# Performance work log

Measured on AMD Instinct MI355X. Metric: run time of the kernel, lower is better.

The kernel has to match this reference:

```python
import jax, jax.numpy as jnp
import numpy as np

D_MODEL = 1024
NUM_HEADS = 16
D_K = D_MODEL // NUM_HEADS
ROPE_BASE = 10000.0


def _rotate_half(x):
    # interleaved pairs: (x0, x1) -> (-x1, x0)
    x1 = x[..., ::2]
    x2 = x[..., 1::2]
    return jnp.stack((-x2, x1), axis=-1).reshape(x.shape)


def _rope(q, k):
    seq_len = q.shape[-2]
    freqs = ROPE_BASE ** (jnp.arange(0, D_K, 2, dtype=q.dtype) / D_K)  # [D_K/2]
    angles = jnp.arange(seq_len, dtype=q.dtype)[:, None] / freqs[None, :]  # [S, D_K/2]
    sin = jnp.repeat(jnp.sin(angles), 2, axis=-1)[None, None]  # [1,1,S,D_K]
    cos = jnp.repeat(jnp.cos(angles), 2, axis=-1)[None, None]
    return q * cos + _rotate_half(q) * sin, k * cos + _rotate_half(k) * sin


def setup_inputs() -> dict:
    key = jax.random.key(0)
    ks = jax.random.split(key, 9)
    B, S, D = 2, 2048, D_MODEL
    s = 1.0 / np.sqrt(D)
    inp = {
        "x": jax.random.normal(ks[0], (B, S, D), dtype=jnp.float32),
        "wq": jax.random.uniform(ks[1], (D, D), jnp.float32, -s, s),
        "bq": jax.random.uniform(ks[2], (D,), jnp.float32, -s, s),
        "wk": jax.random.uniform(ks[3], (D, D), jnp.float32, -s, s),
        "bk": jax.random.uniform(ks[4], (D,), jnp.float32, -s, s),
        "wv": jax.random.uniform(ks[5], (D, D), jnp.float32, -s, s),
        "bv": jax.random.uniform(ks[6], (D,), jnp.float32, -s, s),
        "wo": jax.random.uniform(ks[7], (D, D), jnp.float32, -s, s),
        "bo": jax.random.uniform(ks[8], (D,), jnp.float32, -s, s),
    }
    return inp


def reference(x, wq, bq, wk, bk, wv, bv, wo, bo):
    B, S, D = x.shape
    H, dk = NUM_HEADS, D_K
    # torch Linear: y = x @ W.T + b
    Q = (x @ wq.T + bq).reshape(B, S, H, dk).transpose(0, 2, 1, 3)  # [B,H,S,dk]
    K = (x @ wk.T + bk).reshape(B, S, H, dk).transpose(0, 2, 1, 3)
    V = (x @ wv.T + bv).reshape(B, S, H, dk).transpose(0, 2, 1, 3)
    Q, K = _rope(Q, K)
    score = jnp.einsum("bhqd,bhkd->bhqk", Q, K) / jnp.sqrt(jnp.asarray(dk, x.dtype))
    attn_w = jax.nn.softmax(score, axis=-1)
    out = jnp.einsum("bhqk,bhkd->bhqd", attn_w, V)  # [B,H,S,dk]
    out = out.transpose(0, 2, 1, 3).reshape(B, S, D)
    return out @ wo.T + bo
```

## Files before the change

kernel.cpp:

```cpp
#include <hip/hip_runtime.h>
#include <hip/hip_bf16.h>
#include <math.h>

typedef __bf16 bf16_t;
typedef __bf16 bf16x4_t __attribute__((ext_vector_type(4)));
typedef __bf16 bf16x8_t __attribute__((ext_vector_type(8)));
typedef float  f32x4_t  __attribute__((ext_vector_type(4)));

#define SEQ 2048
#define DM  1024
#define NH  16
#define DK  64
#define ROPE_C 0.4152410118609203f
#define EXP_C (1.4426950408889634f / 8.0f)

#define GLD16(gp, lp) \
  __builtin_amdgcn_global_load_lds((__attribute__((address_space(1))) const void*)(gp), \
                                   (__attribute__((address_space(3))) void*)(lp), 16, 0, 0)

__global__ __launch_bounds__(256)
void prep_kernel(const float* __restrict__ x,  const float* __restrict__ wq,
                 const float* __restrict__ wk, const float* __restrict__ wv,
                 const float* __restrict__ wo, bf16_t* __restrict__ dst,
                 float2* __restrict__ lut) {
  if (blockIdx.x < 8192) {
    int i = blockIdx.x * 256 + threadIdx.x;
    const float* s;
    if (i < 1048576) {
      s = x + (size_t)i * 4;
    } else {
      int j = i - 1048576;
      int w = j >> 18;
      const float* base = (w == 0) ? wq : (w == 1) ? wk : (w == 2) ? wv : wo;
      s = base + (size_t)(j & 262143) * 4;
    }
    float4 v = *(const float4*)s;
    bf16x4_t o;
    o.x = (bf16_t)v.x; o.y = (bf16_t)v.y; o.z = (bf16_t)v.z; o.w = (bf16_t)v.w;
    ((bf16x4_t*)dst)[i] = o;
  } else {
    int i = (blockIdx.x - 8192) * 256 + threadIdx.x;
    int s = i >> 5, f = i & 31;
    float ang = (float)s * exp2f(-ROPE_C * (float)f);
    float sn, cs;
    sincosf(ang, &sn, &cs);
    lut[i] = make_float2(sn, cs);
  }
}

__global__ __launch_bounds__(256, 3)
void gemm_qkv(const bf16_t* __restrict__ A, const bf16_t* __restrict__ Wq,
              const bf16_t* __restrict__ Wk, const bf16_t* __restrict__ Wv,
              const float* __restrict__ bq, const float* __restrict__ bk,
              const float* __restrict__ bv, const float2* __restrict__ lut,
              bf16_t* __restrict__ Qb, bf16_t* __restrict__ Kb,
              bf16_t* __restrict__ Vtb) {
  const int K = 1024;
  __shared__ bf16_t As[128 * 64];
  __shared__ bf16_t Bs[128 * 64];

  const int tid  = threadIdx.x;
  const int w    = tid >> 6;
  const int lane = tid & 63;
  const int quad = lane >> 4;
  const int lrow = lane & 15;
  const int wm = (w >> 1) * 64, wn = (w & 1) * 64;

  const int srow8 = lane >> 3;
  const int scolz = (((lane & 7) ^ (lane >> 3)) * 8);

  const int id   = blockIdx.x;
  const int xcd  = id & 7;
  const int rank = id >> 3;
  const int isV  = rank >= 64;

  const bf16_t* Ablk;
  const bf16_t* Bblk;
  int bmQK = 0, bnl = 0, isK = 0, bmF = 0, bnT = 0;
  if (!isV) {
    const int q = xcd * 64 + rank;
    bmQK = q >> 4;
    const int bn = q & 15;
    isK = bn >> 3;
    bnl = bn & 7;
    Ablk = A + (size_t)(bmQK * 128) * K;
    Bblk = (isK ? Wk : Wq) + (size_t)(bnl * 128) * K;
  } else {
    const int v = xcd * 32 + (rank - 64);
    bnT = v >> 3;
    bmF = v & 7;
    Ablk = Wv + (size_t)(bmF * 128) * K;
    Bblk = A + (size_t)(bnT * 128) * K;
  }

  f32x4_t acc[4][4] = {};

  for (int k0 = 0; k0 < K; k0 += 64) {
#pragma unroll
    for (int i = 0; i < 4; i++) {
      GLD16(&Ablk[(size_t)(w * 32 + i * 8 + srow8) * K + k0 + scolz], &As[(w * 32 + i * 8) * 64]);
      GLD16(&Bblk[(size_t)(w * 32 + i * 8 + srow8) * K + k0 + scolz], &Bs[(w * 32 + i * 8) * 64]);
    }
    __syncthreads();

#pragma unroll
    for (int kk = 0; kk < 2; kk++) {
      const int gsw = (((kk << 2) | quad) ^ (lrow & 7)) * 8;
      bf16x8_t af[4], bf[4];
#pragma unroll
      for (int mi = 0; mi < 4; mi++)
        af[mi] = *(const bf16x8_t*)(&As[(wm + mi * 16 + lrow) * 64 + gsw]);
#pragma unroll
      for (int ni = 0; ni < 4; ni++)
        bf[ni] = *(const bf16x8_t*)(&Bs[(wn + ni * 16 + lrow) * 64 + gsw]);
#pragma unroll
      for (int mi = 0; mi < 4; mi++)
#pragma unroll
        for (int ni = 0; ni < 4; ni++)
          acc[mi][ni] = __builtin_amdgcn_mfma_f32_16x16x32_bf16(af[mi], bf[ni], acc[mi][ni], 0, 0, 0);
    }
    __syncthreads();
  }

  if (!isV) {
    const int brow = bmQK * 128 + wm;
    const int cbase = bnl * 128 + wn;
    const float* bias = isK ? bk : bq;
    bf16_t* D = isK ? Kb : Qb;

#pragma unroll
    for (int ni = 0; ni < 4; ni++) {
      const int col = cbase + ni * 16 + lrow;
      const float bvv = bias[col];
      const int t = col & 63;
      const int h = col >> 6;
      const int fidx = t >> 1;
#pragma unroll
      for (int mi = 0; mi < 4; mi++) {
        f32x4_t v = acc[mi][ni];
#pragma unroll
        for (int r = 0; r < 4; r++) {
          const int row = brow + mi * 16 + quad * 4 + r;
          const int s = row & (SEQ - 1);
          float val = v[r] + bvv;
          const float2 sc = lut[s * 32 + fidx];
          const float pv = __shfl_xor(val, 1);
          val = (t & 1) ? (val * sc.y + pv * sc.x) : (val * sc.y - pv * sc.x);
          const int b = row >> 11;
          const size_t o = (((size_t)(b * NH + h) * SEQ) + s) * DK + t;
          D[o] = (bf16_t)val;
        }
      }
    }
  } else {
    const int fbase = bmF * 128 + wm;
    const int tbase = bnT * 128 + wn;

#pragma unroll
    for (int ni = 0; ni < 4; ni++) {
      const int t = tbase + ni * 16 + lrow;
      const int b = t >> 11;
      const int s = t & (SEQ - 1);
#pragma unroll
      for (int mi = 0; mi < 4; mi++) {
        f32x4_t v = acc[mi][ni];
        const int f = fbase + mi * 16 + quad * 4;
        const int h = f >> 6, d = f & 63;
#pragma unroll
        for (int r = 0; r < 4; r++)
          Vtb[((size_t)((b * NH + h) * DK + d + r)) * SEQ + s] = (bf16_t)(v[r] + bv[f + r]);
      }
    }
  }
}

__global__ __launch_bounds__(256)
void gemm_out(const bf16_t* __restrict__ A, const bf16_t* __restrict__ Bw,
              const float* __restrict__ bias, float* __restrict__ D) {
  const int K = 1024;
  __shared__ bf16_t As[128 * 32];
  __shared__ bf16_t Bs[64 * 32];

  const int tid  = threadIdx.x;
  const int w    = tid >> 6;
  const int lane = tid & 63;
  const int quad = lane >> 4;
  const int lrow = lane & 15;
  const int wm = (w >> 1) * 64, wn = (w & 1) * 32;

  const int id  = blockIdx.x;
  const int swz = (id & 7) * 64 + (id >> 3);
  const int bm  = swz >> 4;
  const int bn  = swz & 15;

  const bf16_t* Ablk = A  + (size_t)(bm * 128) * K;
  const bf16_t* Bblk = Bw + (size_t)(bn * 64) * K;

  f32x4_t acc[4][2] = {};

  const int srow = lane >> 2;
  const int scol = (lane & 3) * 8;

  for (int k0 = 0; k0 < K; k0 += 32) {
    GLD16(&Ablk[(size_t)(w * 32 + srow) * K + k0 + scol],      &As[(w * 32) * 32]);
    GLD16(&Ablk[(size_t)(w * 32 + 16 + srow) * K + k0 + scol], &As[(w * 32 + 16) * 32]);
    GLD16(&Bblk[(size_t)(w * 16 + srow) * K + k0 + scol],      &Bs[(w * 16) * 32]);
    __syncthreads();

    bf16x8_t af[4], bf[2];
#pragma unroll
    for (int mi = 0; mi < 4; mi++)
      af[mi] = *(const bf16x8_t*)(&As[(wm + mi * 16 + lrow) * 32 + quad * 8]);
#pragma unroll
    for (int ni = 0; ni < 2; ni++)
      bf[ni] = *(const bf16x8_t*)(&Bs[(wn + ni * 16 + lrow) * 32 + quad * 8]);
#pragma unroll
    for (int mi = 0; mi < 4; mi++)
#pragma unroll
      for (int ni = 0; ni < 2; ni++)
        acc[mi][ni] = __builtin_amdgcn_mfma_f32_16x16x32_bf16(af[mi], bf[ni], acc[mi][ni], 0, 0, 0);
    __syncthreads();
  }

#pragma unroll
  for (int ni = 0; ni < 2; ni++) {
    const int col = bn * 64 + wn + ni * 16 + lrow;
    const float bvv = bias[col];
#pragma unroll
    for (int mi = 0; mi < 4; mi++) {
      f32x4_t v = acc[mi][ni];
#pragma unroll
      for (int r = 0; r < 4; r++) {
        const int row = bm * 128 + wm + mi * 16 + quad * 4 + r;
        D[(size_t)row * DM + col] = v[r] + bvv;
      }
    }
  }
}

__global__ __launch_bounds__(512)
void attn_kernel(const bf16_t* __restrict__ Q, const bf16_t* __restrict__ K,
                 const bf16_t* __restrict__ Vt, bf16_t* __restrict__ AO) {
  __shared__ bf16_t Ks[128 * 64];
  __shared__ bf16_t Vs[64 * 128];

  const int tid  = threadIdx.x;
  const int w    = tid >> 6;
  const int lane = tid & 63;
  const int quad = lane >> 4;
  const int lrow = lane & 15;

  const int id  = blockIdx.x;
  const int swz = (id & 7) * 64 + (id >> 3);
  const int bh  = swz >> 4;
  const int q0  = (swz & 15) * 128 + w * 16;

  const bf16_t* Qh  = Q  + (size_t)bh * SEQ * DK;
  const bf16_t* Kh  = K  + (size_t)bh * SEQ * DK;
  const bf16_t* Vth = Vt + (size_t)bh * DK * SEQ;

  bf16x8_t qf[2];
#pragma unroll
  for (int c = 0; c < 2; c++) {
    bf16x8_t t = *(const bf16x8_t*)(&Qh[(size_t)(q0 + lrow) * DK + c * 32 + quad * 8]);
#pragma unroll
    for (int i = 0; i < 8; i++) t[i] = (bf16_t)((float)t[i] * EXP_C);
    qf[c] = t;
  }

  f32x4_t accO[4] = {};
  float lsum = 0.f;

  const int krow = tid >> 2;
  const int kcol = (tid & 3) * 16;
  const int kg0  = (tid & 3) * 2;
  const int vrow = tid >> 3;
  const int vcol = (tid & 7) * 16;

  const int kw0 = krow * 64 + ((kg0       ^ (krow & 7)) << 3);
  const int kw1 = krow * 64 + (((kg0 + 1) ^ (krow & 7)) << 3);
  const int vb  = (vcol >> 5) * 4;
  const int vh  = ((vcol >> 4) & 1) * 4;
  const int vsw = vrow & 15;
  const int vw0 = vrow * 128 + (((vb + 0) ^ vsw) << 3) + vh;
  const int vw1 = vrow * 128 + (((vb + 1) ^ vsw) << 3) + vh;
  const int vw2 = vrow * 128 + (((vb + 2) ^ vsw) << 3) + vh;
  const int vw3 = vrow * 128 + (((vb + 3) ^ vsw) << 3) + vh;

  uint4 kr0 = *(const uint4*)(&Kh[(size_t)krow * DK + kcol]);
  uint4 kr1 = *(const uint4*)(&Kh[(size_t)krow * DK + kcol + 8]);
  uint4 vr0 = *(const uint4*)(&Vth[(size_t)vrow * SEQ + vcol]);
  uint4 vr1 = *(const uint4*)(&Vth[(size_t)vrow * SEQ + vcol + 8]);

  for (int kt = 0; kt < SEQ / 128; ++kt) {
    *(uint4*)(&Ks[kw0]) = kr0;
    *(uint4*)(&Ks[kw1]) = kr1;
    *(uint2*)(&Vs[vw0]) = make_uint2(vr0.x, vr0.y);
    *(uint2*)(&Vs[vw1]) = make_uint2(vr0.z, vr0.w);
    *(uint2*)(&Vs[vw2]) = make_uint2(vr1.x, vr1.y);
    *(uint2*)(&Vs[vw3]) = make_uint2(vr1.z, vr1.w);
    __syncthreads();

    if (kt + 1 < SEQ / 128) {
      const int kb = (kt + 1) * 128;
      kr0 = *(const uint4*)(&Kh[(size_t)(kb + krow) * DK + kcol]);
      kr1 = *(const uint4*)(&Kh[(size_t)(kb + krow) * DK + kcol + 8]);
      vr0 = *(const uint4*)(&Vth[(size_t)vrow * SEQ + kb + vcol]);
      vr1 = *(const uint4*)(&Vth[(size_t)vrow * SEQ + kb + vcol + 8]);
    }

    __builtin_amdgcn_s_setprio(1);
#pragma unroll
    for (int c2 = 0; c2 < 4; ++c2) {
      uint2 pk[2];
#pragma unroll
      for (int kk2 = 0; kk2 < 2; ++kk2) {
        const int kk = c2 * 2 + kk2;
        const int krd = (kk * 16 + lrow) * 64;
        bf16x8_t kf0 = *(const bf16x8_t*)(&Ks[krd + ((quad       ^ (lrow & 7)) << 3)]);
        bf16x8_t kf1 = *(const bf16x8_t*)(&Ks[krd + (((quad + 4) ^ (lrow & 7)) << 3)]);
        f32x4_t z = {};
        z = __builtin_amdgcn_mfma_f32_16x16x32_bf16(kf0, qf[0], z, 0, 0, 0);
        z = __builtin_amdgcn_mfma_f32_16x16x32_bf16(kf1, qf[1], z, 0, 0, 0);
        const float p0 = __builtin_amdgcn_exp2f(z[0]), p1 = __builtin_amdgcn_exp2f(z[1]);
        const float p2 = __builtin_amdgcn_exp2f(z[2]), p3 = __builtin_amdgcn_exp2f(z[3]);
        lsum += (p0 + p1) + (p2 + p3);
        pk[kk2].x = __builtin_amdgcn_perm(__builtin_bit_cast(unsigned, p1),
                                          __builtin_bit_cast(unsigned, p0), 0x07060302u);
        pk[kk2].y = __builtin_amdgcn_perm(__builtin_bit_cast(unsigned, p3),
                                          __builtin_bit_cast(unsigned, p2), 0x07060302u);
      }
      uint4 pfu;
      pfu.x = pk[0].x; pfu.y = pk[0].y; pfu.z = pk[1].x; pfu.w = pk[1].y;
      bf16x8_t pf = __builtin_bit_cast(bf16x8_t, pfu);
#pragma unroll
      for (int nt = 0; nt < 4; ++nt) {
        bf16x8_t vf = *(const bf16x8_t*)(
            &Vs[(nt * 16 + lrow) * 128 + ((((c2 << 2) | quad) ^ lrow) << 3)]);
        accO[nt] = __builtin_amdgcn_mfma_f32_16x16x32_bf16(pf, vf, accO[nt], 0, 0, 0);
      }
    }
    __builtin_amdgcn_s_setprio(0);
    __syncthreads();
  }

  lsum += __shfl_xor(lsum, 16);
  lsum += __shfl_xor(lsum, 32);
  float linv[4];
#pragma unroll
  for (int r = 0; r < 4; r++)
    linv[r] = 1.0f / __shfl(lsum, quad * 4 + r);

  const int b = bh >> 4, h = bh & 15;
#pragma unroll
  for (int nt = 0; nt < 4; nt++)
#pragma unroll
    for (int r = 0; r < 4; r++) {
      const int srowq = q0 + quad * 4 + r;
      const float val = accO[nt][r] * linv[r];
      const size_t o = ((size_t)(b * SEQ + srowq)) * DM + h * DK + nt * 16 + lrow;
      AO[o] = (bf16_t)val;
    }
}

extern "C" void kernel_launch(void* const* d_in, const int* in_sizes, int n_in,
                              void* d_out, int out_size, void* d_ws, size_t ws_size,
                              hipStream_t stream) {
  const float* x  = (const float*)d_in[0];
  const float* wq = (const float*)d_in[1];
  const float* bq = (const float*)d_in[2];
  const float* wk = (const float*)d_in[3];
  const float* bk = (const float*)d_in[4];
  const float* wv = (const float*)d_in[5];
  const float* bv = (const float*)d_in[6];
  const float* wo = (const float*)d_in[7];
  const float* bo = (const float*)d_in[8];
  float* out = (float*)d_out;

  char* ws = (char*)d_ws;
  bf16_t* xb   = (bf16_t*)(ws);
  bf16_t* wqb  = (bf16_t*)(ws + 8388608);
  bf16_t* wkb  = (bf16_t*)(ws + 10485760);
  bf16_t* wvb  = (bf16_t*)(ws + 12582912);
  bf16_t* wob  = (bf16_t*)(ws + 14680064);
  bf16_t* Qb   = (bf16_t*)(ws + 16777216);
  bf16_t* Kb   = (bf16_t*)(ws + 25165824);
  bf16_t* Vtb  = (bf16_t*)(ws + 33554432);
  bf16_t* AOb  = (bf16_t*)(ws + 41943040);
  float2* lut  = (float2*)(ws + 50331648);

  prep_kernel<<<8448, 256, 0, stream>>>(x, wq, wk, wv, wo, xb, lut);

  gemm_qkv<<<768, 256, 0, stream>>>(xb, wqb, wkb, wvb, bq, bk, bv, lut, Qb, Kb, Vtb);

  attn_kernel<<<512, 512, 0, stream>>>(Qb, Kb, Vtb, AOb);

  gemm_out<<<512, 256, 0, stream>>>(AOb, wob, bo, out);
}
```

Before: 179.0 us.

## Deepen gemm_out K tile with swizzled LDS and halve attention block size

The output projection GEMM now stages a 64-wide K slice per iteration with XOR-swizzled LDS layout. This halves the number of barrier pairs and is meant to avoid bank conflicts. The attention kernel moves from 512-thread blocks covering 128 queries to 256-thread blocks covering 64 queries, with each thread loading twice as much K/V per tile. This doubles the grid and allows more resident blocks per CU, at the cost of twice the total K/V tile loads across blocks.

Measured after the change: 183.4 us. 1.02x slower.

```diff
diff --git a/kernel.cpp b/kernel.cpp
--- a/kernel.cpp
+++ b/kernel.cpp
@@ -178,8 +178,8 @@
 void gemm_out(const bf16_t* __restrict__ A, const bf16_t* __restrict__ Bw,
               const float* __restrict__ bias, float* __restrict__ D) {
   const int K = 1024;
-  __shared__ bf16_t As[128 * 32];
-  __shared__ bf16_t Bs[64 * 32];
+  __shared__ bf16_t As[128 * 64];
+  __shared__ bf16_t Bs[64 * 64];
 
   const int tid  = threadIdx.x;
   const int w    = tid >> 6;
@@ -188,6 +188,9 @@
   const int lrow = lane & 15;
   const int wm = (w >> 1) * 64, wn = (w & 1) * 32;
 
+  const int srow8 = lane >> 3;
+  const int scolz = (((lane & 7) ^ (lane >> 3)) * 8);
+
   const int id  = blockIdx.x;
   const int swz = (id & 7) * 64 + (id >> 3);
   const int bm  = swz >> 4;
@@ -198,27 +201,31 @@
 
   f32x4_t acc[4][2] = {};
 
-  const int srow = lane >> 2;
-  const int scol = (lane & 3) * 8;
-
-  for (int k0 = 0; k0 < K; k0 += 32) {
-    GLD16(&Ablk[(size_t)(w * 32 + srow) * K + k0 + scol],      &As[(w * 32) * 32]);
-    GLD16(&Ablk[(size_t)(w * 32 + 16 + srow) * K + k0 + scol], &As[(w * 32 + 16) * 32]);
-    GLD16(&Bblk[(size_t)(w * 16 + srow) * K + k0 + scol],      &Bs[(w * 16) * 32]);
-    __syncthreads();
-
-    bf16x8_t af[4], bf[2];
-#pragma unroll
-    for (int mi = 0; mi < 4; mi++)
-      af[mi] = *(const bf16x8_t*)(&As[(wm + mi * 16 + lrow) * 32 + quad * 8]);
-#pragma unroll
-    for (int ni = 0; ni < 2; ni++)
-      bf[ni] = *(const bf16x8_t*)(&Bs[(wn + ni * 16 + lrow) * 32 + quad * 8]);
-#pragma unroll
-    for (int mi = 0; mi < 4; mi++)
+  for (int k0 = 0; k0 < K; k0 += 64) {
+#pragma unroll
+    for (int i = 0; i < 4; i++)
+      GLD16(&Ablk[(size_t)(w * 32 + i * 8 + srow8) * K + k0 + scolz], &As[(w * 32 + i * 8) * 64]);
+#pragma unroll
+    for (int i = 0; i < 2; i++)
+      GLD16(&Bblk[(size_t)(w * 16 + i * 8 + srow8) * K + k0 + scolz], &Bs[(w * 16 + i * 8) * 64]);
+    __syncthreads();
+
+#pragma unroll
+    for (int kk = 0; kk < 2; kk++) {
+      const int gsw = (((kk << 2) | quad) ^ (lrow & 7)) * 8;
+      bf16x8_t af[4], bf[2];
+#pragma unroll
+      for (int mi = 0; mi < 4; mi++)
+        af[mi] = *(const bf16x8_t*)(&As[(wm + mi * 16 + lrow) * 64 + gsw]);
 #pragma unroll
       for (int ni = 0; ni < 2; ni++)
-        acc[mi][ni] = __builtin_amdgcn_mfma_f32_16x16x32_bf16(af[mi], bf[ni], acc[mi][ni], 0, 0, 0);
+        bf[ni] = *(const bf16x8_t*)(&Bs[(wn + ni * 16 + lrow) * 64 + gsw]);
+#pragma unroll
+      for (int mi = 0; mi < 4; mi++)
+#pragma unroll
+        for (int ni = 0; ni < 2; ni++)
+          acc[mi][ni] = __builtin_amdgcn_mfma_f32_16x16x32_bf16(af[mi], bf[ni], acc[mi][ni], 0, 0, 0);
+    }
     __syncthreads();
   }
 
@@ -238,7 +245,7 @@
   }
 }
 
-__global__ __launch_bounds__(512)
+__global__ __launch_bounds__(256, 4)
 void attn_kernel(const bf16_t* __restrict__ Q, const bf16_t* __restrict__ K,
                  const bf16_t* __restrict__ Vt, bf16_t* __restrict__ AO) {
   __shared__ bf16_t Ks[128 * 64];
@@ -251,9 +258,9 @@
   const int lrow = lane & 15;
 
   const int id  = blockIdx.x;
-  const int swz = (id & 7) * 64 + (id >> 3);
-  const int bh  = swz >> 4;
-  const int q0  = (swz & 15) * 128 + w * 16;
+  const int swz = (id & 7) * 128 + (id >> 3);
+  const int bh  = swz >> 5;
+  const int q0  = (swz & 31) * 64 + w * 16;
 
   const bf16_t* Qh  = Q  + (size_t)bh * SEQ * DK;
   const bf16_t* Kh  = K  + (size_t)bh * SEQ * DK;
@@ -271,42 +278,60 @@
   f32x4_t accO[4] = {};
   float lsum = 0.f;
 
-  const int krow = tid >> 2;
-  const int kcol = (tid & 3) * 16;
-  const int kg0  = (tid & 3) * 2;
-  const int vrow = tid >> 3;
-  const int vcol = (tid & 7) * 16;
-
-  const int kw0 = krow * 64 + ((kg0       ^ (krow & 7)) << 3);
-  const int kw1 = krow * 64 + (((kg0 + 1) ^ (krow & 7)) << 3);
-  const int vb  = (vcol >> 5) * 4;
-  const int vh  = ((vcol >> 4) & 1) * 4;
-  const int vsw = vrow & 15;
-  const int vw0 = vrow * 128 + (((vb + 0) ^ vsw) << 3) + vh;
-  const int vw1 = vrow * 128 + (((vb + 1) ^ vsw) << 3) + vh;
-  const int vw2 = vrow * 128 + (((vb + 2) ^ vsw) << 3) + vh;
-  const int vw3 = vrow * 128 + (((vb + 3) ^ vsw) << 3) + vh;
+  const int krow = tid >> 1;
+  const int kcol = (tid & 1) * 32;
+  const int kg0  = (tid & 1) * 4;
+  const int ksw  = krow & 7;
+  const int kwr  = krow * 64;
+  const int kw0 = kwr + (((kg0 + 0) ^ ksw) << 3);
+  const int kw1 = kwr + (((kg0 + 1) ^ ksw) << 3);
+  const int kw2 = kwr + (((kg0 + 2) ^ ksw) << 3);
+  const int kw3 = kwr + (((kg0 + 3) ^ ksw) << 3);
+
+  const int vrow = tid >> 2;
+  const int vcol = (tid & 3) * 32;
+  const int vG   = (tid & 3) * 4;
+  const int vsw  = vrow & 15;
+  const int vwr  = vrow * 128;
+  const int vw0 = vwr + (((vG + 0) ^ vsw) << 3);
+  const int vw1 = vwr + (((vG + 1) ^ vsw) << 3);
+  const int vw2 = vwr + (((vG + 2) ^ vsw) << 3);
+  const int vw3 = vwr + (((vG + 3) ^ vsw) << 3);
 
   uint4 kr0 = *(const uint4*)(&Kh[(size_t)krow * DK + kcol]);
   uint4 kr1 = *(const uint4*)(&Kh[(size_t)krow * DK + kcol + 8]);
+  uint4 kr2 = *(const uint4*)(&Kh[(size_t)krow * DK + kcol + 16]);
+  uint4 kr3 = *(const uint4*)(&Kh[(size_t)krow * DK + kcol + 24]);
   uint4 vr0 = *(const uint4*)(&Vth[(size_t)vrow * SEQ + vcol]);
   uint4 vr1 = *(const uint4*)(&Vth[(size_t)vrow * SEQ + vcol + 8]);
+  uint4 vr2 = *(const uint4*)(&Vth[(size_t)vrow * SEQ + vcol + 16]);
+  uint4 vr3 = *(const uint4*)(&Vth[(size_t)vrow * SEQ + vcol + 24]);
 
   for (int kt = 0; kt < SEQ / 128; ++kt) {
     *(uint4*)(&Ks[kw0]) = kr0;
     *(uint4*)(&Ks[kw1]) = kr1;
-    *(uint2*)(&Vs[vw0]) = make_uint2(vr0.x, vr0.y);
-    *(uint2*)(&Vs[vw1]) = make_uint2(vr0.z, vr0.w);
-    *(uint2*)(&Vs[vw2]) = make_uint2(vr1.x, vr1.y);
-    *(uint2*)(&Vs[vw3]) = make_uint2(vr1.z, vr1.w);
+    *(uint4*)(&Ks[kw2]) = kr2;
+    *(uint4*)(&Ks[kw3]) = kr3;
+    *(uint2*)(&Vs[vw0])     = make_uint2(vr0.x, vr0.y);
+    *(uint2*)(&Vs[vw1])     = make_uint2(vr0.z, vr0.w);
+    *(uint2*)(&Vs[vw2])     = make_uint2(vr1.x, vr1.y);
+    *(uint2*)(&Vs[vw3])     = make_uint2(vr1.z, vr1.w);
+    *(uint2*)(&Vs[vw0 + 4]) = make_uint2(vr2.x, vr2.y);
+    *(uint2*)(&Vs[vw1 + 4]) = make_uint2(vr2.z, vr2.w);
+    *(uint2*)(&Vs[vw2 + 4]) = make_uint2(vr3.x, vr3.y);
+    *(uint2*)(&Vs[vw3 + 4]) = make_uint2(vr3.z, vr3.w);
     __syncthreads();
 
     if (kt + 1 < SEQ / 128) {
       const int kb = (kt + 1) * 128;
       kr0 = *(const uint4*)(&Kh[(size_t)(kb + krow) * DK + kcol]);
       kr1 = *(const uint4*)(&Kh[(size_t)(kb + krow) * DK + kcol + 8]);
+      kr2 = *(const uint4*)(&Kh[(size_t)(kb + krow) * DK + kcol + 16]);
+      kr3 = *(const uint4*)(&Kh[(size_t)(kb + krow) * DK + kcol + 24]);
       vr0 = *(const uint4*)(&Vth[(size_t)vrow * SEQ + kb + vcol]);
       vr1 = *(const uint4*)(&Vth[(size_t)vrow * SEQ + kb + vcol + 8]);
+      vr2 = *(const uint4*)(&Vth[(size_t)vrow * SEQ + kb + vcol + 16]);
+      vr3 = *(const uint4*)(&Vth[(size_t)vrow * SEQ + kb + vcol + 24]);
     }
 
     __builtin_amdgcn_s_setprio(1);
@@ -393,7 +418,7 @@
 
   gemm_qkv<<<768, 256, 0, stream>>>(xb, wqb, wkb, wvb, bq, bk, bv, lut, Qb, Kb, Vtb);
 
-  attn_kernel<<<512, 512, 0, stream>>>(Qb, Kb, Vtb, AOb);
+  attn_kernel<<<1024, 256, 0, stream>>>(Qb, Kb, Vtb, AOb);
 
   gemm_out<<<512, 256, 0, stream>>>(AOb, wob, bo, out);
 }
```

## Double-buffer attention K/V tiles and widen output GEMM k-step with swizzled LDS

Applied to the files above, without the earlier changes.

The attention kernel now keeps two LDS buffers for K and V. The next tile is written into the spare buffer after compute, so each iteration needs one barrier instead of two, and global-to-LDS staging overlaps with MFMA work. Separately, the output projection GEMM loads 64-wide k-slices per iteration with an XOR-swizzled layout, which halves the number of barriers and spreads LDS bank accesses. LDS use doubles in both kernels, which may reduce occupancy.

Result: slower. 184.8 us (+3.2%).

```diff
diff --git a/kernel.cpp b/kernel.cpp
--- a/kernel.cpp
+++ b/kernel.cpp
@@ -178,8 +178,8 @@
 void gemm_out(const bf16_t* __restrict__ A, const bf16_t* __restrict__ Bw,
               const float* __restrict__ bias, float* __restrict__ D) {
   const int K = 1024;
-  __shared__ bf16_t As[128 * 32];
-  __shared__ bf16_t Bs[64 * 32];
+  __shared__ bf16_t As[128 * 64];
+  __shared__ bf16_t Bs[64 * 64];
 
   const int tid  = threadIdx.x;
   const int w    = tid >> 6;
@@ -188,6 +188,9 @@
   const int lrow = lane & 15;
   const int wm = (w >> 1) * 64, wn = (w & 1) * 32;
 
+  const int srow8 = lane >> 3;
+  const int scolz = (((lane & 7) ^ (lane >> 3)) * 8);
+
   const int id  = blockIdx.x;
   const int swz = (id & 7) * 64 + (id >> 3);
   const int bm  = swz >> 4;
@@ -198,27 +201,31 @@
 
   f32x4_t acc[4][2] = {};
 
-  const int srow = lane >> 2;
-  const int scol = (lane & 3) * 8;
-
-  for (int k0 = 0; k0 < K; k0 += 32) {
-    GLD16(&Ablk[(size_t)(w * 32 + srow) * K + k0 + scol],      &As[(w * 32) * 32]);
-    GLD16(&Ablk[(size_t)(w * 32 + 16 + srow) * K + k0 + scol], &As[(w * 32 + 16) * 32]);
-    GLD16(&Bblk[(size_t)(w * 16 + srow) * K + k0 + scol],      &Bs[(w * 16) * 32]);
+  for (int k0 = 0; k0 < K; k0 += 64) {
+#pragma unroll
+    for (int i = 0; i < 4; i++)
+      GLD16(&Ablk[(size_t)(w * 32 + i * 8 + srow8) * K + k0 + scolz], &As[(w * 32 + i * 8) * 64]);
+#pragma unroll
+    for (int i = 0; i < 2; i++)
+      GLD16(&Bblk[(size_t)(w * 16 + i * 8 + srow8) * K + k0 + scolz], &Bs[(w * 16 + i * 8) * 64]);
     __syncthreads();
 
-    bf16x8_t af[4], bf[2];
-#pragma unroll
-    for (int mi = 0; mi < 4; mi++)
-      af[mi] = *(const bf16x8_t*)(&As[(wm + mi * 16 + lrow) * 32 + quad * 8]);
-#pragma unroll
-    for (int ni = 0; ni < 2; ni++)
-      bf[ni] = *(const bf16x8_t*)(&Bs[(wn + ni * 16 + lrow) * 32 + quad * 8]);
-#pragma unroll
-    for (int mi = 0; mi < 4; mi++)
+#pragma unroll
+    for (int kk = 0; kk < 2; kk++) {
+      const int gsw = (((kk << 2) | quad) ^ (lrow & 7)) * 8;
+      bf16x8_t af[4], bf[2];
+#pragma unroll
+      for (int mi = 0; mi < 4; mi++)
+        af[mi] = *(const bf16x8_t*)(&As[(wm + mi * 16 + lrow) * 64 + gsw]);
 #pragma unroll
       for (int ni = 0; ni < 2; ni++)
-        acc[mi][ni] = __builtin_amdgcn_mfma_f32_16x16x32_bf16(af[mi], bf[ni], acc[mi][ni], 0, 0, 0);
+        bf[ni] = *(const bf16x8_t*)(&Bs[(wn + ni * 16 + lrow) * 64 + gsw]);
+#pragma unroll
+      for (int mi = 0; mi < 4; mi++)
+#pragma unroll
+        for (int ni = 0; ni < 2; ni++)
+          acc[mi][ni] = __builtin_amdgcn_mfma_f32_16x16x32_bf16(af[mi], bf[ni], acc[mi][ni], 0, 0, 0);
+    }
     __syncthreads();
   }
 
@@ -241,8 +248,8 @@
 __global__ __launch_bounds__(512)
 void attn_kernel(const bf16_t* __restrict__ Q, const bf16_t* __restrict__ K,
                  const bf16_t* __restrict__ Vt, bf16_t* __restrict__ AO) {
-  __shared__ bf16_t Ks[128 * 64];
-  __shared__ bf16_t Vs[64 * 128];
+  __shared__ bf16_t Ks[2][128 * 64];
+  __shared__ bf16_t Vs[2][64 * 128];
 
   const int tid  = threadIdx.x;
   const int w    = tid >> 6;
@@ -291,17 +298,20 @@
   uint4 kr1 = *(const uint4*)(&Kh[(size_t)krow * DK + kcol + 8]);
   uint4 vr0 = *(const uint4*)(&Vth[(size_t)vrow * SEQ + vcol]);
   uint4 vr1 = *(const uint4*)(&Vth[(size_t)vrow * SEQ + vcol + 8]);
-
+  *(uint4*)(&Ks[0][kw0]) = kr0;
+  *(uint4*)(&Ks[0][kw1]) = kr1;
+  *(uint2*)(&Vs[0][vw0]) = make_uint2(vr0.x, vr0.y);
+  *(uint2*)(&Vs[0][vw1]) = make_uint2(vr0.z, vr0.w);
+  *(uint2*)(&Vs[0][vw2]) = make_uint2(vr1.x, vr1.y);
+  *(uint2*)(&Vs[0][vw3]) = make_uint2(vr1.z, vr1.w);
+  __syncthreads();
+
+#pragma unroll 2
   for (int kt = 0; kt < SEQ / 128; ++kt) {
-    *(uint4*)(&Ks[kw0]) = kr0;
-    *(uint4*)(&Ks[kw1]) = kr1;
-    *(uint2*)(&Vs[vw0]) = make_uint2(vr0.x, vr0.y);
-    *(uint2*)(&Vs[vw1]) = make_uint2(vr0.z, vr0.w);
-    *(uint2*)(&Vs[vw2]) = make_uint2(vr1.x, vr1.y);
-    *(uint2*)(&Vs[vw3]) = make_uint2(vr1.z, vr1.w);
-    __syncthreads();
-
-    if (kt + 1 < SEQ / 128) {
+    const int cur = kt & 1, nxt = cur ^ 1;
+    const bool more = (kt + 1 < SEQ / 128);
+
+    if (more) {
       const int kb = (kt + 1) * 128;
       kr0 = *(const uint4*)(&Kh[(size_t)(kb + krow) * DK + kcol]);
       kr1 = *(const uint4*)(&Kh[(size_t)(kb + krow) * DK + kcol + 8]);
@@ -317,8 +327,8 @@
       for (int kk2 = 0; kk2 < 2; ++kk2) {
         const int kk = c2 * 2 + kk2;
         const int krd = (kk * 16 + lrow) * 64;
-        bf16x8_t kf0 = *(const bf16x8_t*)(&Ks[krd + ((quad       ^ (lrow & 7)) << 3)]);
-        bf16x8_t kf1 = *(const bf16x8_t*)(&Ks[krd + (((quad + 4) ^ (lrow & 7)) << 3)]);
+        bf16x8_t kf0 = *(const bf16x8_t*)(&Ks[cur][krd + ((quad       ^ (lrow & 7)) << 3)]);
+        bf16x8_t kf1 = *(const bf16x8_t*)(&Ks[cur][krd + (((quad + 4) ^ (lrow & 7)) << 3)]);
         f32x4_t z = {};
         z = __builtin_amdgcn_mfma_f32_16x16x32_bf16(kf0, qf[0], z, 0, 0, 0);
         z = __builtin_amdgcn_mfma_f32_16x16x32_bf16(kf1, qf[1], z, 0, 0, 0);
@@ -336,11 +346,20 @@
 #pragma unroll
       for (int nt = 0; nt < 4; ++nt) {
         bf16x8_t vf = *(const bf16x8_t*)(
-            &Vs[(nt * 16 + lrow) * 128 + ((((c2 << 2) | quad) ^ lrow) << 3)]);
+            &Vs[cur][(nt * 16 + lrow) * 128 + ((((c2 << 2) | quad) ^ lrow) << 3)]);
         accO[nt] = __builtin_amdgcn_mfma_f32_16x16x32_bf16(pf, vf, accO[nt], 0, 0, 0);
       }
     }
     __builtin_amdgcn_s_setprio(0);
+
+    if (more) {
+      *(uint4*)(&Ks[nxt][kw0]) = kr0;
+      *(uint4*)(&Ks[nxt][kw1]) = kr1;
+      *(uint2*)(&Vs[nxt][vw0]) = make_uint2(vr0.x, vr0.y);
+      *(uint2*)(&Vs[nxt][vw1]) = make_uint2(vr0.z, vr0.w);
+      *(uint2*)(&Vs[nxt][vw2]) = make_uint2(vr1.x, vr1.y);
+      *(uint2*)(&Vs[nxt][vw3]) = make_uint2(vr1.z, vr1.w);
+    }
     __syncthreads();
   }
 
```
